# Performance work log

Measured on AMD Instinct MI355X. Metric: run time of the kernel, lower is better.

## Reference

```python
import jax, jax.numpy as jnp
import numpy as np
from jax import lax

B, S, H, V, J, K = 8, 512, 768, 35004, 30, 9
PAD = 0

def setup_inputs() -> dict:
    key = jax.random.key(0)
    ks = jax.random.split(key, 12)
    std = 0.02
    return {
        'x': jax.random.randint(ks[0], (B, S), 0, V),
        'decoder_input': jax.random.normal(ks[1], (B, J, H), jnp.float32),
        'encoder_output': jax.random.normal(ks[2], (B, S, H), jnp.float32),
        'hidden': jax.random.normal(ks[3], (1, B, H), jnp.float32),
        'teacher': jax.random.randint(ks[4], (B, J, K), 0, V),
        'max_len': K,
        'embed': jax.random.normal(ks[5], (V, H), jnp.float32) * std,
        'w_ih': jax.random.normal(ks[6], (3 * H, H), jnp.float32) * std,
        'w_hh': jax.random.normal(ks[7], (3 * H, H), jnp.float32) * std,
        'b_ih': jnp.zeros((3 * H,), jnp.float32),
        'b_hh': jnp.zeros((3 * H,), jnp.float32),
        'wg_w': jax.random.normal(ks[8], (1, 3 * H), jnp.float32) * std,
        'wg_b': jnp.zeros((1,), jnp.float32),
    }

def gru_cell(w, h, w_ih, w_hh, b_ih, b_hh):
    # PyTorch GRU gate order: reset, update, new
    gi = w @ w_ih.T + b_ih          # [B,3H]
    gh = h @ w_hh.T + b_hh          # [B,3H]
    ir, iz, inn = jnp.split(gi, 3, axis=-1)
    hr, hz, hn = jnp.split(gh, 3, axis=-1)
    r = jax.nn.sigmoid(ir + hr)
    z = jax.nn.sigmoid(iz + hz)
    n = jnp.tanh(inn + r * hn)
    return (1.0 - z) * n + z * h

def reference(x, decoder_input, encoder_output, hidden, teacher, max_len,
              embed, w_ih, w_hh, b_ih, b_hh, wg_w, wg_b):
    mask = (x == PAD)                      # [B,S]
    batch_ix = jnp.arange(x.shape[0])[:, None]

    def tok_step(carry, teach_t):
        w, h = carry                       # w,h: [B,H]; teach_t: [B]
        h = gru_cell(w, h, w_ih, w_hh, b_ih, b_hh)
        logits_hist = jnp.einsum('bsh,bh->bs', encoder_output, h)
        logits_hist = jnp.where(mask, -1e9, logits_hist)
        a_hist = jax.nn.softmax(logits_hist, axis=-1)          # [B,S]
        a_vocab = jax.nn.softmax(h @ embed.T, axis=-1)         # [B,V]
        context = jnp.einsum('bs,bsh->bh', a_hist, encoder_output)
        p_gen = jax.nn.sigmoid(
            jnp.concatenate([w, h, context], axis=-1) @ wg_w.T + wg_b)  # [B,1]
        p_ctx = jnp.zeros_like(a_vocab).at[batch_ix, x].add(a_hist)     # scatter_add pointer copy
        p_final = p_gen * a_vocab + (1.0 - p_gen) * p_ctx
        w_next = embed[teach_t]            # teacher forcing (dropout omitted: eval mode)
        return (w_next, h), p_final

    def slot_step(h, slot_in):
        w0, teach_j = slot_in              # w0: [B,H]; teach_j: [K,B]
        (_, h), p = lax.scan(tok_step, (w0, h), teach_j)
        return h, p                        # p: [K,B,V]

    h0 = hidden[0]                                      # [B,H]
    slots = jnp.swapaxes(decoder_input, 0, 1)           # [J,B,H]
    teach = jnp.transpose(teacher, (1, 2, 0))           # [J,K,B]
    _, outs = lax.scan(slot_step, h0, (slots, teach))   # [J,K,B,V]
    return jnp.transpose(outs, (2, 0, 1, 3))            # [B,J,K,V]
```

## Files before the change

### kernel.cpp

```cpp
#include <hip/hip_runtime.h>
#include <hip/hip_bf16.h>

typedef _Float16 f16;
typedef _Float16 f16x8 __attribute__((ext_vector_type(8)));
typedef _Float16 f16x4v __attribute__((ext_vector_type(4)));
typedef _Float16 h2 __attribute__((ext_vector_type(2)));
typedef float f32x4 __attribute__((ext_vector_type(4)));
typedef unsigned ui4v __attribute__((ext_vector_type(4)));
typedef unsigned long long ull;

#define B_ 8
#define S_ 512
#define H_ 768
#define V_ 35004
#define J_ 30
#define K_ 9
#define R_ 2160
#define H3 2304
#define VMT 17
#define VNT 274
#define CASTB 864


__global__ void k_prep(const float* __restrict__ emb, const float* __restrict__ dec,
                       const int* __restrict__ teacher, f16* __restrict__ Wall,
                       const float* __restrict__ wih, f16* __restrict__ wih16) {
    int r = blockIdx.x;
    if (r < R_) {
        int b = r / 270, s = r % 270, j = s / 9, t = s % 9;
        const float* src = (t == 0) ? dec + ((long)b * J_ + j) * H_
                                    : emb + (long)teacher[((long)b * J_ + j) * K_ + (t - 1)] * H_;
        f16* dst = Wall + (long)r * H_;
        for (int c = threadIdx.x; c < H_; c += 256) dst[c] = (f16)src[c];
    } else {
        const long n = (long)H3 * H_;
        for (long i = (long)(r - R_) * 256 + threadIdx.x; i < n; i += (long)CASTB * 256)
            wih16[i] = (f16)wih[i];
    }
}

__global__ void k_init_h(const float* __restrict__ hidden, ull* __restrict__ hbuf) {
    int i = blockIdx.x * 256 + threadIdx.x;
    if (i < B_ * H_) {
        int b = i / H_, u = i % H_;
        hbuf[(long)b * 1536 + u] = (ull)__float_as_uint(hidden[i]);
        hbuf[(long)b * 1536 + 768 + u] = 0;
    }
}

typedef const __attribute__((address_space(1))) unsigned GASU;
typedef __attribute__((address_space(3))) unsigned LASU;
__device__ __forceinline__ void gld16(const f16* g, f16* l) {
    __builtin_amdgcn_global_load_lds((GASU*)g, (LASU*)l, 16, 0, 0);
}

template <int MODE>
__global__ __launch_bounds__(256) void k_gemm(const f16* __restrict__ A, const f16* __restrict__ Bm,
                                              float* __restrict__ C, const float* __restrict__ bias,
                                              int M, int N, int K, long sA, long sB, long sC) {
    A += (long)blockIdx.z * sA;
    Bm += (long)blockIdx.z * sB;
    C += (long)blockIdx.z * sC;
    const int m0 = blockIdx.y * 128, n0 = blockIdx.x * 128;
    __shared__ f16 As[128 * 32];
    __shared__ f16 Bs[128 * 32];
    const int tid = threadIdx.x, lane = tid & 63, wave = tid >> 6;
    const int wm = wave >> 1, wn = wave & 1;
    const int fr = lane & 15, kg = lane >> 4;
    f32x4 acc[4][4] = {};
    const int idxu = wave * 128;
    const int i0 = idxu + lane, i1 = idxu + 64 + lane;
    const int r0 = i0 >> 2, k80 = i0 & 3;
    const int r1 = i1 >> 2, k81 = i1 & 3;
    int ga0 = m0 + r0; if (ga0 >= M) ga0 = M - 1;
    int ga1 = m0 + r1; if (ga1 >= M) ga1 = M - 1;
    int gb0 = n0 + r0; if (gb0 >= N) gb0 = N - 1;
    int gb1 = n0 + r1; if (gb1 >= N) gb1 = N - 1;
    const f16* pa0 = A + (long)ga0 * K + k80 * 8;
    const f16* pa1 = A + (long)ga1 * K + k81 * 8;
    const f16* pb0 = Bm + (long)gb0 * K + k80 * 8;
    const f16* pb1 = Bm + (long)gb1 * K + k81 * 8;
    for (int kt = 0; kt < K; kt += 32) {
        gld16(pa0 + kt, As + idxu * 8);
        gld16(pa1 + kt, As + idxu * 8 + 512);
        gld16(pb0 + kt, Bs + idxu * 8);
        gld16(pb1 + kt, Bs + idxu * 8 + 512);
        __syncthreads();
        f16x8 af[4], bf[4];
#pragma unroll
        for (int m = 0; m < 4; ++m) af[m] = *(const f16x8*)(As + (wm * 64 + m * 16 + fr) * 32 + kg * 8);
#pragma unroll
        for (int n = 0; n < 4; ++n) bf[n] = *(const f16x8*)(Bs + (wn * 64 + n * 16 + fr) * 32 + kg * 8);
#pragma unroll
        for (int m = 0; m < 4; ++m)
#pragma unroll
            for (int n = 0; n < 4; ++n)
                acc[m][n] = __builtin_amdgcn_mfma_f32_16x16x32_f16(af[m], bf[n], acc[m][n], 0, 0, 0);
        __syncthreads();
    }
    const int crow = m0 + wm * 64 + (lane >> 4) * 4;
    const int ccol = n0 + wn * 64 + fr;
#pragma unroll
    for (int n = 0; n < 4; ++n) {
        int col = ccol + n * 16;
        if (col >= N) continue;
        float bv = (MODE == 1) ? bias[col] : 0.f;
#pragma unroll
        for (int m = 0; m < 4; ++m) {
#pragma unroll
            for (int q = 0; q < 4; ++q) {
                int row = crow + m * 16 + q;
                if (row < M) C[(long)row * N + col] = acc[m][n][q] + bv;
            }
        }
    }
}

__global__ __launch_bounds__(256) void k_attn3(const f16* __restrict__ Ahi, const f16* __restrict__ Alo,
                                               const f16* __restrict__ Bhi, const f16* __restrict__ Blo,
                                               float* __restrict__ C, int M, int N, int K,
                                               long sA, long sB, long sC) {
    const long za = (long)blockIdx.z * sA, zb = (long)blockIdx.z * sB;
    C += (long)blockIdx.z * sC;
    const int m0 = blockIdx.y * 128, n0 = blockIdx.x * 128;
    __shared__ f16 As[128 * 32];
    __shared__ f16 Bs[128 * 32];
    const int tid = threadIdx.x, lane = tid & 63, wave = tid >> 6;
    const int wm = wave >> 1, wn = wave & 1;
    const int fr = lane & 15, kg = lane >> 4;
    f32x4 acc[4][4] = {};
    const int idxu = wave * 128;
    const int i0 = idxu + lane, i1 = idxu + 64 + lane;
    const int r0 = i0 >> 2, k80 = i0 & 3;
    const int r1 = i1 >> 2, k81 = i1 & 3;
    int ga0 = m0 + r0; if (ga0 >= M) ga0 = M - 1;
    int ga1 = m0 + r1; if (ga1 >= M) ga1 = M - 1;
    int gb0 = n0 + r0; if (gb0 >= N) gb0 = N - 1;
    int gb1 = n0 + r1; if (gb1 >= N) gb1 = N - 1;
    const long oa0 = (long)ga0 * K + k80 * 8, oa1 = (long)ga1 * K + k81 * 8;
    const long ob0 = (long)gb0 * K + k80 * 8, ob1 = (long)gb1 * K + k81 * 8;
    for (int ph = 0; ph < 3; ++ph) {
        const f16* Ap = (ph == 2 ? Alo : Ahi) + za;
        const f16* Bp = (ph == 1 ? Blo : Bhi) + zb;
        for (int kt = 0; kt < K; kt += 32) {
            gld16(Ap + oa0 + kt, As + idxu * 8);
            gld16(Ap + oa1 + kt, As + idxu * 8 + 512);
            gld16(Bp + ob0 + kt, Bs + idxu * 8);
            gld16(Bp + ob1 + kt, Bs + idxu * 8 + 512);
            __syncthreads();
            f16x8 af[4], bf[4];
#pragma unroll
            for (int m = 0; m < 4; ++m) af[m] = *(const f16x8*)(As + (wm * 64 + m * 16 + fr) * 32 + kg * 8);
#pragma unroll
            for (int n = 0; n < 4; ++n) bf[n] = *(const f16x8*)(Bs + (wn * 64 + n * 16 + fr) * 32 + kg * 8);
#pragma unroll
            for (int m = 0; m < 4; ++m)
#pragma unroll
                for (int n = 0; n < 4; ++n)
                    acc[m][n] = __builtin_amdgcn_mfma_f32_16x16x32_f16(af[m], bf[n], acc[m][n], 0, 0, 0);
            __syncthreads();
        }
    }
    const int crow = m0 + wm * 64 + (lane >> 4) * 4;
    const int ccol = n0 + wn * 64 + fr;
#pragma unroll
    for (int n = 0; n < 4; ++n) {
        int col = ccol + n * 16;
        if (col >= N) continue;
#pragma unroll
        for (int m = 0; m < 4; ++m) {
#pragma unroll
            for (int q = 0; q < 4; ++q) {
                int row = crow + m * 16 + q;
                if (row < M) C[(long)row * N + col] = acc[m][n][q];
            }
        }
    }
}

__global__ __launch_bounds__(256) void k_vocab(const f16* __restrict__ A, const f16* __restrict__ Bm,
                                               float* __restrict__ C, float* __restrict__ psum) {
    const int M = R_, N = V_, K = H_;
    const int nwg = VMT * VNT;
    int lin = blockIdx.x;
    int q8 = nwg / 8, r8 = nwg % 8;
    int xcd = lin & 7, idx = lin >> 3;
    int newlin = (xcd < r8) ? xcd * (q8 + 1) + idx : r8 * (q8 + 1) + (xcd - r8) * q8 + idx;
    int mt = newlin % VMT, nt = newlin / VMT;
    const int m0 = mt * 128, n0 = nt * 128;
    __shared__ f16 As[128 * 32];
    __shared__ f16 Bs[128 * 32];
    __shared__ float rpart[2][128];
    const int tid = threadIdx.x, lane = tid & 63, wave = tid >> 6;
    const int wm = wave >> 1, wn = wave & 1;
    const int fr = lane & 15, kg = lane >> 4;
    f32x4 acc[4][4] = {};
    const int idxu = wave * 128;
    const int i0 = idxu + lane, i1 = idxu + 64 + lane;
    const int r0 = i0 >> 2, k80 = i0 & 3;
    const int r1 = i1 >> 2, k81 = i1 & 3;
    int ga0 = m0 + r0; if (ga0 >= M) ga0 = M - 1;
    int ga1 = m0 + r1; if (ga1 >= M) ga1 = M - 1;
    int gb0 = n0 + r0; if (gb0 >= N) gb0 = N - 1;
    int gb1 = n0 + r1; if (gb1 >= N) gb1 = N - 1;
    const f16* pa0 = A + (long)ga0 * K + k80 * 8;
    const f16* pa1 = A + (long)ga1 * K + k81 * 8;
    const f16* pb0 = Bm + (long)gb0 * K + k80 * 8;
    const f16* pb1 = Bm + (long)gb1 * K + k81 * 8;
    for (int kt = 0; kt < K; kt += 32) {
        gld16(pa0 + kt, As + idxu * 8);
        gld16(pa1 + kt, As + idxu * 8 + 512);
        gld16(pb0 + kt, Bs + idxu * 8);
        gld16(pb1 + kt, Bs + idxu * 8 + 512);
        __syncthreads();
        f16x8 af[4], bf[4];
#pragma unroll
        for (int m = 0; m < 4; ++m) af[m] = *(const f16x8*)(As + (wm * 64 + m * 16 + fr) * 32 + kg * 8);
#pragma unroll
        for (int n = 0; n < 4; ++n) bf[n] = *(const f16x8*)(Bs + (wn * 64 + n * 16 + fr) * 32 + kg * 8);
#pragma unroll
        for (int m = 0; m < 4; ++m)
#pragma unroll
            for (int n = 0; n < 4; ++n)
                acc[m][n] = __builtin_amdgcn_mfma_f32_16x16x32_f16(af[m], bf[n], acc[m][n], 0, 0, 0);
        __syncthreads();
    }
    const int crow = m0 + wm * 64 + (lane >> 4) * 4;
    const int ccol = n0 + wn * 64 + fr;
    float rs[4][4];
#pragma unroll
    for (int m = 0; m < 4; ++m)
#pragma unroll
        for (int q = 0; q < 4; ++q) rs[m][q] = 0.f;
#pragma unroll
    for (int n = 0; n < 4; ++n) {
        int col = ccol + n * 16;
        if (col >= N) continue;
#pragma unroll
        for (int m = 0; m < 4; ++m) {
#pragma unroll
            for (int q = 0; q < 4; ++q) {
                int row = crow + m * 16 + q;
                if (row < M) {
                    float e = __expf(acc[m][n][q]);
                    C[(long)row * N + col] = e;
                    rs[m][q] += e;
                }
            }
        }
    }
#pragma unroll
    for (int m = 0; m < 4; ++m)
#pragma unroll
        for (int q = 0; q < 4; ++q) {
            float v = rs[m][q];
            v += __shfl_xor(v, 1);
            v += __shfl_xor(v, 2);
            v += __shfl_xor(v, 4);
            v += __shfl_xor(v, 8);
            rs[m][q] = v;
        }
    if ((lane & 15) == 0) {
#pragma unroll
        for (int m = 0; m < 4; ++m)
#pragma unroll
            for (int q = 0; q < 4; ++q)
                rpart[wn][wm * 64 + (lane >> 4) * 4 + m * 16 + q] = rs[m][q];
    }
    __syncthreads();
    if (tid < 128) {
        int row = m0 + tid;
        if (row < M) psum[(long)nt * M + row] = rpart[0][tid] + rpart[1][tid];
    }
}

__device__ __forceinline__ float fd2(unsigned hv, unsigned wv, float acc) {
#if __has_builtin(__builtin_amdgcn_fdot2)
    return __builtin_amdgcn_fdot2(__builtin_bit_cast(h2, hv), __builtin_bit_cast(h2, wv), acc, false);
#else
    h2 a = __builtin_bit_cast(h2, hv), b = __builtin_bit_cast(h2, wv);
    return acc + (float)a.x * (float)b.x + (float)a.y * (float)b.y;
#endif
}

__global__ __launch_bounds__(256, 1) void k_gru(const float* __restrict__ gi,
                                                const float* __restrict__ whh,
                                                const float* __restrict__ bhh,
                                                ull* hbuf,
                                                f16* __restrict__ Hhi, f16* __restrict__ Hlo,
                                                const float* __restrict__ emb, f16* __restrict__ emb16,
                                                const float* __restrict__ enc, f16* __restrict__ ehi,
                                                f16* __restrict__ elo, f16* __restrict__ encT) {
    __shared__ ui4v wsvu[9216];
    __shared__ __align__(16) f16 hsf[768];
    __shared__ float part[2][8][32][3];
    const int tid = threadIdx.x;
    if (blockIdx.x >= 192) {
        const long pt = (long)(blockIdx.x - 192) * 256 + tid;
        const long n4 = (long)V_ * H_ / 4;
        for (long i = pt; i < n4; i += 64 * 256) {
            f32x4 v = ((const f32x4*)emb)[i];
            f16x4v r = {(f16)v.x, (f16)v.y, (f16)v.z, (f16)v.w};
            ((f16x4v*)emb16)[i] = r;
        }
        const long n4e = (long)B_ * S_ * H_ / 4;
        for (long i = pt; i < n4e; i += 64 * 256) {
            f32x4 v = ((const f32x4*)enc)[i];
            f16 h0 = (f16)v.x, h1 = (f16)v.y, h2v = (f16)v.z, h3 = (f16)v.w;
            f16x4v hv = {h0, h1, h2v, h3};
            ((f16x4v*)ehi)[i] = hv;
            f16x4v lv = {(f16)(v.x - (float)h0), (f16)(v.y - (float)h1),
                         (f16)(v.z - (float)h2v), (f16)(v.w - (float)h3)};
            ((f16x4v*)elo)[i] = lv;
        }
        float* tl = (float*)wsvu;
        for (int t = blockIdx.x - 192; t < 8 * 8 * 12; t += 64) {
            int ht = t % 12, st = (t / 12) % 8, bb = t / 96;
            __syncthreads();
#pragma unroll
            for (int k = 0; k < 16; ++k) {
                int i = tid + k * 256;
                int sl = i >> 6, hl = i & 63;
                tl[sl * 65 + hl] = enc[((long)bb * S_ + st * 64 + sl) * H_ + ht * 64 + hl];
            }
            __syncthreads();
#pragma unroll
            for (int k = 0; k < 16; ++k) {
                int i = tid + k * 256;
                int hl = i >> 6, sl = i & 63;
                encT[((long)bb * H_ + ht * 64 + hl) * S_ + st * 64 + sl] = (f16)tl[sl * 65 + hl];
            }
        }
        return;
    }
    const int chain = blockIdx.x / 24;
    const int blk = blockIdx.x % 24;
    const int u0 = blk * 32;
    for (int idx = tid; idx < 9216; idx += 256) {
        int uu = idx & 31, k8 = (idx >> 5) % 96, g = idx / (96 * 32);
        const float* src = whh + (long)(g * H_ + u0 + uu) * H_ + k8 * 8;
        f32x4 a = *(const f32x4*)src;
        f32x4 b2 = *(const f32x4*)(src + 4);
        f16x8 pk = {(f16)a.x, (f16)a.y, (f16)a.z, (f16)a.w,
                    (f16)b2.x, (f16)b2.y, (f16)b2.z, (f16)b2.w};
        wsvu[idx] = __builtin_bit_cast(ui4v, pk);
    }
    float b_r = 0.f, b_z = 0.f, b_n = 0.f;
    if (tid < 32) {
        int c = u0 + tid;
        b_r = bhh[c];
        b_z = bhh[H_ + c];
        b_n = bhh[2 * H_ + c];
    }
    __syncthreads();
    const int u = tid & 31, q = tid >> 5, lane = tid & 63;
    const int pw = (tid >> 6) * 192 + lane;
    ui4v wreg[3][12];
#pragma unroll
    for (int g = 0; g < 3; ++g)
#pragma unroll
        for (int i = 0; i < 12; ++i)
            wreg[g][i] = wsvu[(g * 96 + q * 12 + i) * 32 + u];
    ull* base = hbuf + (long)chain * 1536;
    const bool fin = (tid < 32);
    float g0 = 0.f, g1 = 0.f, g2v = 0.f;
    if (fin) {
        const float* gp = gi + (long)chain * 270 * H3;
        int c = u0 + tid;
        g0 = gp[c];
        g1 = gp[H_ + c];
        g2v = gp[2 * H_ + c];
    }
    for (int s = 0; s < 270; ++s) {
        const ull* rb = base + (s & 1) * 768;
        ull* wb = base + ((s + 1) & 1) * 768;
        const unsigned want = (unsigned)s;
        ull v0, v1, v2, vh = 0;
        for (;;) {
            v0 = __hip_atomic_load(rb + pw, __ATOMIC_RELAXED, __HIP_MEMORY_SCOPE_AGENT);
            v1 = __hip_atomic_load(rb + pw + 64, __ATOMIC_RELAXED, __HIP_MEMORY_SCOPE_AGENT);
            v2 = __hip_atomic_load(rb + pw + 128, __ATOMIC_RELAXED, __HIP_MEMORY_SCOPE_AGENT);
            bool ok = ((unsigned)(v0 >> 32) == want) & ((unsigned)(v1 >> 32) == want) &
                      ((unsigned)(v2 >> 32) == want);
            if (fin) {
                vh = __hip_atomic_load(rb + u0 + tid, __ATOMIC_RELAXED, __HIP_MEMORY_SCOPE_AGENT);
                ok &= ((unsigned)(vh >> 32) == want);
            }
            if (ok) break;
        }
        hsf[pw] = (f16)__uint_as_float((unsigned)v0);
        hsf[pw + 64] = (f16)__uint_as_float((unsigned)v1);
        hsf[pw + 128] = (f16)__uint_as_float((unsigned)v2);
        __builtin_amdgcn_wave_barrier();
        float ar = 0.f, az = 0.f, an = 0.f;
#pragma unroll
        for (int i = 0; i < 12; ++i) {
            ui4v hv = *(const ui4v*)(&hsf[(q * 12 + i) * 8]);
            ui4v wr = wreg[0][i], wz = wreg[1][i], wn = wreg[2][i];
            ar = fd2(hv.x, wr.x, ar); ar = fd2(hv.y, wr.y, ar);
            ar = fd2(hv.z, wr.z, ar); ar = fd2(hv.w, wr.w, ar);
            az = fd2(hv.x, wz.x, az); az = fd2(hv.y, wz.y, az);
            az = fd2(hv.z, wz.z, az); az = fd2(hv.w, wz.w, az);
            an = fd2(hv.x, wn.x, an); an = fd2(hv.y, wn.y, an);
            an = fd2(hv.z, wn.z, an); an = fd2(hv.w, wn.w, an);
        }
        const int par = s & 1;
        part[par][q][u][0] = ar;
        part[par][q][u][1] = az;
        part[par][q][u][2] = an;
        __syncthreads();
        if (fin) {
            float gr = b_r, gz = b_z, gn = b_n;
#pragma unroll
            for (int qq = 0; qq < 8; ++qq) {
                gr += part[par][qq][tid][0];
                gz += part[par][qq][tid][1];
                gn += part[par][qq][tid][2];
            }
            float hold = __uint_as_float((unsigned)vh);
            float rg = 1.f / (1.f + __expf(-(g0 + gr)));
            float zg = 1.f / (1.f + __expf(-(g1 + gz)));
            float xa = g2v + rg * gn;
            float e2 = __expf(-2.f * xa);
            float ng = (1.f - e2) / (1.f + e2);
            float hnew = (1.f - zg) * ng + zg * hold;
            int c = u0 + tid;
            ull wvv = ((ull)(unsigned)(s + 1) << 32) | (ull)__float_as_uint(hnew);
            __hip_atomic_store(wb + c, wvv, __ATOMIC_RELAXED, __HIP_MEMORY_SCOPE_AGENT);
            long row = (long)chain * 270 + s;
            f16 h16 = (f16)hnew;
            Hhi[row * H_ + c] = h16;
            Hlo[row * H_ + c] = (f16)(hnew - (float)h16);
            if (s < 269) {
                const float* gp = gi + ((long)chain * 270 + s + 1) * H3;
                g0 = gp[c];
                g1 = gp[H_ + c];
                g2v = gp[2 * H_ + c];
            }
        }
    }
}

__global__ __launch_bounds__(256) void k_attn_softmax(const float* __restrict__ lg,
                                                      const int* __restrict__ x, f16* __restrict__ ah) {
    __shared__ float red[256];
    int r = blockIdx.x, tid = threadIdx.x;
    int b = r / 270;
    const float* lr = lg + (long)r * S_;
    const int* xb = x + (long)b * S_;
    float v0 = lr[tid];
    if (xb[tid] == 0) v0 = -1e9f;
    float v1 = lr[tid + 256];
    if (xb[tid + 256] == 0) v1 = -1e9f;
    red[tid] = fmaxf(v0, v1);
    __syncthreads();
    for (int o = 128; o > 0; o >>= 1) {
        if (tid < o) red[tid] = fmaxf(red[tid], red[tid + o]);
        __syncthreads();
    }
    float m = red[0];
    __syncthreads();
    float e0 = __expf(v0 - m), e1 = __expf(v1 - m);
    red[tid] = e0 + e1;
    __syncthreads();
    for (int o = 128; o > 0; o >>= 1) {
        if (tid < o) red[tid] += red[tid + o];
        __syncthreads();
    }
    float inv = 1.f / red[0];
    ah[(long)r * S_ + tid] = (f16)(e0 * inv);
    ah[(long)r * S_ + tid + 256] = (f16)(e1 * inv);
}

__global__ __launch_bounds__(256, 1) void k_fin3(float* __restrict__ out,
                                                 const float* __restrict__ psum,
                                                 const f16* __restrict__ Wall,
                                                 const f16* __restrict__ Hhi,
                                                 const f16* __restrict__ Hlo,
                                                 const float* __restrict__ ctx,
                                                 const float* __restrict__ wg,
                                                 const float* __restrict__ wgb,
                                                 const f16* __restrict__ ah,
                                                 const int* __restrict__ x) {
    __shared__ float row[V_];
    __shared__ float red[256], red2[256];
    const int r = blockIdx.x, tid = threadIdx.x;
    const int b = r / 270;
    float a = 0.f;
    for (int i = tid; i < H_; i += 256) {
        a += (float)Wall[(long)r * H_ + i] * wg[i];
        a += ((float)Hhi[(long)r * H_ + i] + (float)Hlo[(long)r * H_ + i]) * wg[H_ + i];
        a += ctx[(long)r * H_ + i] * wg[2 * H_ + i];
    }
    float s = 0.f;
    for (int i = tid; i < VNT; i += 256) s += psum[(long)i * R_ + r];
    red[tid] = s;
    red2[tid] = a;
    __syncthreads();
    for (int o = 128; o > 0; o >>= 1) {
        if (tid < o) {
            red[tid] += red[tid + o];
            red2[tid] += red2[tid + o];
        }
        __syncthreads();
    }
    const float pgv = 1.f / (1.f + __expf(-(red2[0] + wgb[0])));
    const float scale = pgv / red[0];
    float* orow = out + (long)r * V_;
    for (int i = tid; i < V_ / 4; i += 256) {
        f32x4 v = ((const f32x4*)orow)[i];
        v.x *= scale;
        v.y *= scale;
        v.z *= scale;
        v.w *= scale;
        ((f32x4*)row)[i] = v;
    }
    __syncthreads();
    const float om = 1.f - pgv;
    for (int s2 = tid; s2 < S_; s2 += 256) {
        int xv = x[(long)b * S_ + s2];
        if (xv != 0) {
            float av = (float)ah[(long)r * S_ + s2];
            if (av != 0.f) atomicAdd(&row[xv], om * av);
        }
    }
    __syncthreads();
    for (int i = tid; i < V_ / 4; i += 256)
        ((f32x4*)orow)[i] = ((const f32x4*)row)[i];
}

extern "C" void kernel_launch(void* const* d_in, const int* in_sizes, int n_in, void* d_out,
                              int out_size, void* d_ws, size_t ws_size, hipStream_t stream) {
    (void)in_sizes; (void)n_in; (void)out_size; (void)ws_size;
    const int* x = (const int*)d_in[0];
    const float* dec = (const float*)d_in[1];
    const float* enc = (const float*)d_in[2];
    const float* hid = (const float*)d_in[3];
    const int* tea = (const int*)d_in[4];
    const float* emb = (const float*)d_in[6];
    const float* wih = (const float*)d_in[7];
    const float* whh = (const float*)d_in[8];
    const float* bih = (const float*)d_in[9];
    const float* bhh = (const float*)d_in[10];
    const float* wgw = (const float*)d_in[11];
    const float* wgb = (const float*)d_in[12];
    float* out = (float*)d_out;

    char* w = (char*)d_ws;
    size_t off = 0;
    auto alloc = [&](size_t bytes) {
        void* p = w + off;
        off = (off + bytes + 255) & ~(size_t)255;
        return p;
    };
    ull* hbuf = (ull*)alloc(8 * 1536 * 8);
    f16* Wall = (f16*)alloc((size_t)R_ * H_ * 2);
    f16* wih16 = (f16*)alloc((size_t)H3 * H_ * 2);
    float* giA = (float*)alloc((size_t)R_ * H3 * 4);
    f16* Hhi = (f16*)alloc((size_t)R_ * H_ * 2);
    f16* Hlo = (f16*)alloc((size_t)R_ * H_ * 2);
    f16* emb16 = (f16*)alloc((size_t)V_ * H_ * 2);
    f16* ehi = (f16*)alloc((size_t)B_ * S_ * H_ * 2);
    f16* elo = (f16*)alloc((size_t)B_ * S_ * H_ * 2);
    f16* encT = (f16*)alloc((size_t)B_ * H_ * S_ * 2);
    float* lgH = (float*)alloc((size_t)R_ * S_ * 4);
    f16* ah = (f16*)alloc((size_t)R_ * S_ * 2);
    float* ctx = (float*)alloc((size_t)R_ * H_ * 4);
    float* psum = (float*)alloc((size_t)VNT * R_ * 4);

    k_init_h<<<24, 256, 0, stream>>>(hid, hbuf);
    k_prep<<<R_ + CASTB, 256, 0, stream>>>(emb, dec, tea, Wall, wih, wih16);

    {
        dim3 g(H3 / 128, (R_ + 127) / 128, 1);
        k_gemm<1><<<g, 256, 0, stream>>>(Wall, wih16, giA, bih, R_, H3, H_, 0, 0, 0);
    }
    k_gru<<<256, 256, 0, stream>>>(giA, whh, bhh, hbuf, Hhi, Hlo,
                                   emb, emb16, enc, ehi, elo, encT);

    {
        dim3 g(S_ / 128, 3, 8);
        k_attn3<<<g, 256, 0, stream>>>(Hhi, Hlo, ehi, elo, lgH, 270, S_, H_,
                                       270L * H_, (long)S_ * H_, 270L * S_);
    }
    k_attn_softmax<<<R_, 256, 0, stream>>>(lgH, x, ah);
    {
        dim3 g(H_ / 128, 3, 8);
        k_gemm<0><<<g, 256, 0, stream>>>(ah, encT, ctx, nullptr, 270, H_, S_, 270L * S_, (long)H_ * S_, 270L * H_);
    }

    k_vocab<<<VMT * VNT, 256, 0, stream>>>(Hhi, emb16, out, psum);
    k_fin3<<<R_, 256, 0, stream>>>(out, psum, Wall, Hhi, Hlo, ctx, wgw, wgb, ah, x);
}
```

Baseline: 1.117 ms.

## Store vocab exp values as bf16 in reused workspace and split finalize per row

The vocab GEMM now writes exp(logits) as bf16 into a workspace region reclaimed from buffers that are dead by then, instead of fp32 into the output. The finalize kernel reads the bf16 values, scales them, and writes the fp32 output. Each row's finalize is split across two blocks over vocab halves, which halves LDS use and allows two blocks per CU. This removes one fp32 write and read of the large intermediate, at the cost of bf16 rounding error in the probabilities.

```diff
diff --git a/kernel.cpp b/kernel.cpp
--- a/kernel.cpp
+++ b/kernel.cpp
@@ -7,6 +7,7 @@
 typedef _Float16 h2 __attribute__((ext_vector_type(2)));
 typedef float f32x4 __attribute__((ext_vector_type(4)));
 typedef unsigned ui4v __attribute__((ext_vector_type(4)));
+typedef unsigned short u16x4 __attribute__((ext_vector_type(4)));
 typedef unsigned long long ull;
 
 #define B_ 8
@@ -20,6 +21,10 @@
 #define VMT 17
 #define VNT 274
 #define CASTB 864
+#define VH0 17504
+
+#define ALD(p) __hip_atomic_load((p), __ATOMIC_RELAXED, __HIP_MEMORY_SCOPE_AGENT)
+#define AST(p, v) __hip_atomic_store((p), (v), __ATOMIC_RELAXED, __HIP_MEMORY_SCOPE_AGENT)
 
 
 __global__ void k_prep(const float* __restrict__ emb, const float* __restrict__ dec,
@@ -178,8 +183,10 @@
     }
 }
 
+template <int BF16OUT>
 __global__ __launch_bounds__(256) void k_vocab(const f16* __restrict__ A, const f16* __restrict__ Bm,
-                                               float* __restrict__ C, float* __restrict__ psum) {
+                                               float* __restrict__ Cf, unsigned short* __restrict__ Ch,
+                                               float* __restrict__ psum) {
     const int M = R_, N = V_, K = H_;
     const int nwg = VMT * VNT;
     int lin = blockIdx.x;
@@ -243,7 +250,13 @@
                 int row = crow + m * 16 + q;
                 if (row < M) {
                     float e = __expf(acc[m][n][q]);
-                    C[(long)row * N + col] = e;
+                    if (BF16OUT) {
+                        unsigned uu = __float_as_uint(e);
+                        uu += 0x7FFFu + ((uu >> 16) & 1u);
+                        Ch[(long)row * N + col] = (unsigned short)(uu >> 16);
+                    } else {
+                        Cf[(long)row * N + col] = e;
+                    }
                     rs[m][q] += e;
                 }
             }
@@ -377,13 +390,13 @@
         const unsigned want = (unsigned)s;
         ull v0, v1, v2, vh = 0;
         for (;;) {
-            v0 = __hip_atomic_load(rb + pw, __ATOMIC_RELAXED, __HIP_MEMORY_SCOPE_AGENT);
-            v1 = __hip_atomic_load(rb + pw + 64, __ATOMIC_RELAXED, __HIP_MEMORY_SCOPE_AGENT);
-            v2 = __hip_atomic_load(rb + pw + 128, __ATOMIC_RELAXED, __HIP_MEMORY_SCOPE_AGENT);
+            v0 = ALD(rb + pw);
+            v1 = ALD(rb + pw + 64);
+            v2 = ALD(rb + pw + 128);
             bool ok = ((unsigned)(v0 >> 32) == want) & ((unsigned)(v1 >> 32) == want) &
                       ((unsigned)(v2 >> 32) == want);
             if (fin) {
-                vh = __hip_atomic_load(rb + u0 + tid, __ATOMIC_RELAXED, __HIP_MEMORY_SCOPE_AGENT);
+                vh = ALD(rb + u0 + tid);
                 ok &= ((unsigned)(vh >> 32) == want);
             }
             if (ok) break;
@@ -426,7 +439,7 @@
             float hnew = (1.f - zg) * ng + zg * hold;
             int c = u0 + tid;
             ull wvv = ((ull)(unsigned)(s + 1) << 32) | (ull)__float_as_uint(hnew);
-            __hip_atomic_store(wb + c, wvv, __ATOMIC_RELAXED, __HIP_MEMORY_SCOPE_AGENT);
+            AST(wb + c, wvv);
             long row = (long)chain * 270 + s;
             f16 h16 = (f16)hnew;
             Hhi[row * H_ + c] = h16;
@@ -472,8 +485,10 @@
     ah[(long)r * S_ + tid + 256] = (f16)(e1 * inv);
 }
 
-__global__ __launch_bounds__(256, 1) void k_fin3(float* __restrict__ out,
+template <int BF16>
+__global__ __launch_bounds__(256, 2) void k_fin3(float* __restrict__ out,
                                                  const float* __restrict__ psum,
+                                                 const unsigned short* __restrict__ expv,
                                                  const f16* __restrict__ Wall,
                                                  const f16* __restrict__ Hhi,
                                                  const f16* __restrict__ Hlo,
@@ -482,10 +497,13 @@
                                                  const float* __restrict__ wgb,
                                                  const f16* __restrict__ ah,
                                                  const int* __restrict__ x) {
-    __shared__ float row[V_];
+    __shared__ float row[VH0];
     __shared__ float red[256], red2[256];
-    const int r = blockIdx.x, tid = threadIdx.x;
+    const int r = blockIdx.x >> 1, half = blockIdx.x & 1;
+    const int tid = threadIdx.x;
     const int b = r / 270;
+    const int lo = half ? VH0 : 0;
+    const int len = half ? (V_ - VH0) : VH0;
     float a = 0.f;
     for (int i = tid; i < H_; i += 256) {
         a += (float)Wall[(long)r * H_ + i] * wg[i];
@@ -506,32 +524,47 @@
     }
     const float pgv = 1.f / (1.f + __expf(-(red2[0] + wgb[0])));
     const float scale = pgv / red[0];
-    float* orow = out + (long)r * V_;
-    for (int i = tid; i < V_ / 4; i += 256) {
-        f32x4 v = ((const f32x4*)orow)[i];
-        v.x *= scale;
-        v.y *= scale;
-        v.z *= scale;
-        v.w *= scale;
-        ((f32x4*)row)[i] = v;
+    const int n4 = len / 4;
+    if (BF16) {
+        const unsigned short* ep = expv + (long)r * V_ + lo;
+        for (int i = tid; i < n4; i += 256) {
+            u16x4 v = ((const u16x4*)ep)[i];
+            f32x4 o;
+            o.x = __uint_as_float((unsigned)v.x << 16) * scale;
+            o.y = __uint_as_float((unsigned)v.y << 16) * scale;
+            o.z = __uint_as_float((unsigned)v.z << 16) * scale;
+            o.w = __uint_as_float((unsigned)v.w << 16) * scale;
+            ((f32x4*)row)[i] = o;
+        }
+    } else {
+        const float* op = out + (long)r * V_ + lo;
+        for (int i = tid; i < n4; i += 256) {
+            f32x4 v = ((const f32x4*)op)[i];
+            v.x *= scale;
+            v.y *= scale;
+            v.z *= scale;
+            v.w *= scale;
+            ((f32x4*)row)[i] = v;
+        }
     }
     __syncthreads();
     const float om = 1.f - pgv;
     for (int s2 = tid; s2 < S_; s2 += 256) {
         int xv = x[(long)b * S_ + s2];
-        if (xv != 0) {
+        if (xv != 0 && xv >= lo && xv < lo + len) {
             float av = (float)ah[(long)r * S_ + s2];
-            if (av != 0.f) atomicAdd(&row[xv], om * av);
-        }
-    }
-    __syncthreads();
-    for (int i = tid; i < V_ / 4; i += 256)
+            if (av != 0.f) atomicAdd(&row[xv - lo], om * av);
+        }
+    }
+    __syncthreads();
+    float* orow = out + (long)r * V_ + lo;
+    for (int i = tid; i < n4; i += 256)
         ((f32x4*)orow)[i] = ((const f32x4*)row)[i];
 }
 
 extern "C" void kernel_launch(void* const* d_in, const int* in_sizes, int n_in, void* d_out,
                               int out_size, void* d_ws, size_t ws_size, hipStream_t stream) {
-    (void)in_sizes; (void)n_in; (void)out_size; (void)ws_size;
+    (void)in_sizes; (void)n_in; (void)out_size;
     const int* x = (const int*)d_in[0];
     const float* dec = (const float*)d_in[1];
     const float* enc = (const float*)d_in[2];
@@ -555,18 +588,21 @@
     };
     ull* hbuf = (ull*)alloc(8 * 1536 * 8);
     f16* Wall = (f16*)alloc((size_t)R_ * H_ * 2);
-    f16* wih16 = (f16*)alloc((size_t)H3 * H_ * 2);
-    float* giA = (float*)alloc((size_t)R_ * H3 * 4);
     f16* Hhi = (f16*)alloc((size_t)R_ * H_ * 2);
     f16* Hlo = (f16*)alloc((size_t)R_ * H_ * 2);
     f16* emb16 = (f16*)alloc((size_t)V_ * H_ * 2);
+    f16* ah = (f16*)alloc((size_t)R_ * S_ * 2);
+    float* ctx = (float*)alloc((size_t)R_ * H_ * 4);
+    float* psum = (float*)alloc((size_t)VNT * R_ * 4);
+    const size_t deadbase = off;
+    f16* wih16 = (f16*)alloc((size_t)H3 * H_ * 2);
+    float* giA = (float*)alloc((size_t)R_ * H3 * 4);
     f16* ehi = (f16*)alloc((size_t)B_ * S_ * H_ * 2);
     f16* elo = (f16*)alloc((size_t)B_ * S_ * H_ * 2);
     f16* encT = (f16*)alloc((size_t)B_ * H_ * S_ * 2);
     float* lgH = (float*)alloc((size_t)R_ * S_ * 4);
-    f16* ah = (f16*)alloc((size_t)R_ * S_ * 2);
-    float* ctx = (float*)alloc((size_t)R_ * H_ * 4);
-    float* psum = (float*)alloc((size_t)VNT * R_ * 4);
+    unsigned short* expv = (unsigned short*)(w + deadbase);
+    const bool fused = (deadbase + (size_t)R_ * V_ * 2 <= ws_size);
 
     k_init_h<<<24, 256, 0, stream>>>(hid, hbuf);
     k_prep<<<R_ + CASTB, 256, 0, stream>>>(emb, dec, tea, Wall, wih, wih16);
@@ -589,6 +625,11 @@
         k_gemm<0><<<g, 256, 0, stream>>>(ah, encT, ctx, nullptr, 270, H_, S_, 270L * S_, (long)H_ * S_, 270L * H_);
     }
 
-    k_vocab<<<VMT * VNT, 256, 0, stream>>>(Hhi, emb16, out, psum);
-    k_fin3<<<R_, 256, 0, stream>>>(out, psum, Wall, Hhi, Hlo, ctx, wgw, wgb, ah, x);
-}
+    if (fused) {
+        k_vocab<1><<<VMT * VNT, 256, 0, stream>>>(Hhi, emb16, nullptr, expv, psum);
+        k_fin3<1><<<2 * R_, 256, 0, stream>>>(out, psum, expv, Wall, Hhi, Hlo, ctx, wgw, wgb, ah, x);
+    } else {
+        k_vocab<0><<<VMT * VNT, 256, 0, stream>>>(Hhi, emb16, out, nullptr, psum);
+        k_fin3<0><<<2 * R_, 256, 0, stream>>>(out, psum, nullptr, Wall, Hhi, Hlo, ctx, wgw, wgb, ah, x);
+    }
+}
```

Result: faster. 1.002 ms (median of 2 runs) (-10.3%).
